# Kernel optimization log

Measured on AMD Instinct MI355X. Metric: run time of the kernel, lower is better.

The kernel has to match this reference:

```python
import jax, jax.numpy as jnp
import numpy as np

B, D_IN, H, E, TOP_K, NUM_TASKS = 131072, 512, 256, 8, 2, 1


def setup_inputs() -> dict:
    key = jax.random.key(0)
    ks = jax.random.split(key, 14)
    s = 0.02
    return {
        "x": jax.random.normal(ks[0], (B, D_IN), jnp.float32),
        "W_in": jax.random.normal(ks[1], (D_IN, H), jnp.float32) * s,
        "b_in": jnp.zeros((H,), jnp.float32),
        "W1": jax.random.normal(ks[2], (E, H, H), jnp.float32) * s,
        "b1": jnp.zeros((E, H), jnp.float32),
        "W2": jax.random.normal(ks[3], (E, H, H), jnp.float32) * s,
        "b2": jnp.zeros((E, H), jnp.float32),
        "Wg": jax.random.normal(ks[4], (H, E), jnp.float32) * s,
        "bg": jnp.zeros((E,), jnp.float32),
        "Wh1": jax.random.normal(ks[5], (H, H // 2), jnp.float32) * s,
        "bh1": jnp.zeros((H // 2,), jnp.float32),
        "Wh2": jax.random.normal(ks[6], (H // 2, NUM_TASKS), jnp.float32) * s,
        "bh2": jnp.zeros((NUM_TASKS,), jnp.float32),
    }


def reference(x, W_in, b_in, W1, b1, W2, b2, Wg, bg, Wh1, bh1, Wh2, bh2):
    h = x @ W_in + b_in                                   # [B, H]
    gates = jax.nn.softmax(h @ Wg + bg, axis=-1)          # [B, E]
    top_g, top_i = jax.lax.top_k(gates, TOP_K)            # [B, K]
    top_g = top_g / jnp.sum(top_g, axis=-1, keepdims=True)
    # dense all-expert compute (faithful to the original torch.stack)
    e1 = jax.nn.relu(jnp.einsum('bh,ehk->bek', h, W1) + b1)   # [B, E, H]
    eo = jnp.einsum('bek,ekh->beh', e1, W2) + b2              # [B, E, H]
    sel = jnp.take_along_axis(eo, top_i[:, :, None], axis=1)  # [B, K, H]
    out = jnp.einsum('bk,bkh->bh', top_g, sel)                # [B, H]
    y = jax.nn.relu(out @ Wh1 + bh1)                          # [B, H/2]
    return y @ Wh2 + bh2                                      # [B, num_tasks]
```

## Files before the change

kernel.cpp:

```cpp
#include <hip/hip_runtime.h>
#include <stdint.h>


#define NB 131072
#define DIN 512
#define HD 256

typedef short s16x8 __attribute__((ext_vector_type(8)));
typedef float f32x4 __attribute__((ext_vector_type(4)));

__device__ __forceinline__ unsigned short f2bf(float f) {
  uint32_t u = __builtin_bit_cast(uint32_t, f);
  u += 0x7FFFu + ((u >> 16) & 1u);
  return (unsigned short)(u >> 16);
}
__device__ __forceinline__ float bf2f(unsigned short s) {
  uint32_t u = ((uint32_t)s) << 16;
  return __builtin_bit_cast(float, u);
}

__global__ void k_prep_t(const float* __restrict__ Win, const float* __restrict__ W1,
                         const float* __restrict__ W2, const float* __restrict__ Wh1,
                         unsigned short* wt_in, unsigned short* w1t,
                         unsigned short* w2t, unsigned short* wh1t) {
  const int total = 131072 + 524288 + 524288 + 32768;
  for (int idx = blockIdx.x * 256 + threadIdx.x; idx < total; idx += gridDim.x * 256) {
    if (idx < 131072) {
      int n = idx >> 9, d = idx & 511;
      wt_in[idx] = f2bf(Win[d * 256 + n]);
    } else if (idx < 655360) {
      int i = idx - 131072;
      int e = i >> 16, n = (i >> 8) & 255, k = i & 255;
      w1t[i] = f2bf(W1[(e * 256 + k) * 256 + n]);
    } else if (idx < 1179648) {
      int i = idx - 655360;
      int e = i >> 16, n = (i >> 8) & 255, k = i & 255;
      w2t[i] = f2bf(W2[(e * 256 + k) * 256 + n]);
    } else {
      int i = idx - 1179648;
      int j = i >> 8, h = i & 255;
      wh1t[i] = f2bf(Wh1[h * 128 + j]);
    }
  }
}

__global__ void k_prep_gate(const float* __restrict__ Win, const float* __restrict__ Wg,
                            const float* __restrict__ b_in, const float* __restrict__ bg,
                            double* wf, double* bfv) {
  int t = blockIdx.x * 256 + threadIdx.x;
  if (t < 4096) {
    int d = t >> 3, e = t & 7;
    double acc = 0.0;
    for (int h = 0; h < 256; ++h)
      acc += (double)Win[d * 256 + h] * (double)Wg[h * 8 + e];
    wf[t] = acc;
  }
  if (blockIdx.x == 0 && threadIdx.x < 8) {
    int e = threadIdx.x;
    double acc = (double)bg[e];
    for (int h = 0; h < 256; ++h) acc += (double)b_in[h] * (double)Wg[h * 8 + e];
    bfv[e] = acc;
  }
}

__global__ __launch_bounds__(512) void k_hg(const float* __restrict__ x,
                                            const unsigned short* __restrict__ wt_in,
                                            const float* __restrict__ b_in,
                                            const double* __restrict__ wf,
                                            const double* __restrict__ bfv,
                                            unsigned short* __restrict__ hbuf,
                                            float2* __restrict__ g12,
                                            unsigned int* __restrict__ eidx) {
  __shared__ unsigned short xt[128 * 264];
  __shared__ double wfld[4 * 1026];
  const int tid = threadIdx.x;
  const int lane = tid & 63, wid = tid >> 6;
  const int wr = wid >> 2, wc = wid & 3;
  const int row0 = blockIdx.x * 128;

  for (int i = tid; i < 4096; i += 512)
    wfld[(i >> 10) * 1026 + (i & 1023)] = wf[i];

  f32x4 acc[4][4];
#pragma unroll
  for (int mi = 0; mi < 4; ++mi)
#pragma unroll
    for (int ni = 0; ni < 4; ++ni) acc[mi][ni] = (f32x4)0.0f;

  const int arow = wr * 64 + (lane & 15);
  const int bcol0 = wc * 64 + (lane & 15);
  const int koff = (lane >> 4) * 8;

  for (int ks = 0; ks < 2; ++ks) {
    __syncthreads();
#pragma unroll
    for (int i = 0; i < 8; ++i) {
      int flat = tid + i * 512;
      int r = flat >> 5, c8 = flat & 31;
      const float* src = x + (size_t)(row0 + r) * 512 + ks * 256 + c8 * 8;
      f32x4 v0 = *(const f32x4*)src;
      f32x4 v1 = *(const f32x4*)(src + 4);
      s16x8 sv;
      sv[0] = (short)f2bf(v0[0]); sv[1] = (short)f2bf(v0[1]);
      sv[2] = (short)f2bf(v0[2]); sv[3] = (short)f2bf(v0[3]);
      sv[4] = (short)f2bf(v1[0]); sv[5] = (short)f2bf(v1[1]);
      sv[6] = (short)f2bf(v1[2]); sv[7] = (short)f2bf(v1[3]);
      *(s16x8*)&xt[r * 264 + c8 * 8] = sv;
    }
    __syncthreads();
#pragma unroll
    for (int kk = 0; kk < 8; ++kk) {
      int k0 = kk * 32 + koff;
      s16x8 af[4], bfr[4];
#pragma unroll
      for (int mi = 0; mi < 4; ++mi)
        af[mi] = *(const s16x8*)&xt[(arow + mi * 16) * 264 + k0];
#pragma unroll
      for (int ni = 0; ni < 4; ++ni)
        bfr[ni] = *(const s16x8*)(wt_in + (size_t)(bcol0 + ni * 16) * 512 + ks * 256 + k0);
#pragma unroll
      for (int mi = 0; mi < 4; ++mi)
#pragma unroll
        for (int ni = 0; ni < 4; ++ni)
          acc[mi][ni] = __builtin_amdgcn_mfma_f32_16x16x32_bf16(af[mi], bfr[ni], acc[mi][ni], 0, 0, 0);
    }
  }
  const int r4 = (lane >> 4) * 4;
#pragma unroll
  for (int ni = 0; ni < 4; ++ni) {
    int col = wc * 64 + ni * 16 + (lane & 15);
    float bin = b_in[col];
#pragma unroll
    for (int mi = 0; mi < 4; ++mi) {
      int rbase = row0 + wr * 64 + mi * 16 + r4;
#pragma unroll
      for (int j = 0; j < 4; ++j)
        hbuf[(size_t)(rbase + j) * 256 + col] = f2bf(acc[mi][ni][j] + bin);
    }
  }

  const int r = tid >> 2, q = tid & 3;
  double z[8];
#pragma unroll
  for (int e = 0; e < 8; ++e) z[e] = 0.0;
  const float* xrow = x + (size_t)(row0 + r) * 512 + q * 128;
  const double* wq = &wfld[q * 1026];
  for (int dd = 0; dd < 32; ++dd) {
    f32x4 xv = *(const f32x4*)(xrow + dd * 4);
#pragma unroll
    for (int j = 0; j < 4; ++j) {
      double xd = (double)xv[j];
      const double* wrow = wq + (dd * 4 + j) * 8;
#pragma unroll
      for (int e = 0; e < 8; ++e) z[e] += xd * wrow[e];
    }
  }
#pragma unroll
  for (int e = 0; e < 8; ++e) {
    z[e] += __shfl_xor(z[e], 1);
    z[e] += __shfl_xor(z[e], 2);
  }
  if (q == 0) {
#pragma unroll
    for (int e = 0; e < 8; ++e) z[e] += bfv[e];
    int i1 = 0; double m1 = z[0];
#pragma unroll
    for (int e = 1; e < 8; ++e) if (z[e] > m1) { m1 = z[e]; i1 = e; }
    int i2 = -1; double m2 = -1e300;
#pragma unroll
    for (int e = 0; e < 8; ++e) if (e != i1 && z[e] > m2) { m2 = z[e]; i2 = e; }
    double s = exp(m2 - m1);
    int token = row0 + r;
    g12[token] = make_float2((float)(1.0 / (1.0 + s)), (float)(s / (1.0 + s)));
    eidx[token] = (unsigned)(i1 | (i2 << 4));
  }
}

__global__ __launch_bounds__(256) void k_hist(const unsigned int* __restrict__ eidx,
                                              unsigned int* __restrict__ bhist) {
  __shared__ unsigned int wcnt[4][8];
  const int tid = threadIdx.x;
  const int w = tid >> 6, lane = tid & 63;
  unsigned v = eidx[blockIdx.x * 256 + tid];
  int i1 = (int)(v & 15u), i2 = (int)((v >> 4) & 15u);
#pragma unroll
  for (int e = 0; e < 8; ++e) {
    unsigned long long m0 = __ballot(i1 == e);
    unsigned long long m1 = __ballot(i2 == e);
    if (lane == 0) wcnt[w][e] = (unsigned)(__popcll(m0) + __popcll(m1));
  }
  __syncthreads();
  if (tid < 8)
    bhist[blockIdx.x * 8 + tid] =
        wcnt[0][tid] + wcnt[1][tid] + wcnt[2][tid] + wcnt[3][tid];
}

__global__ __launch_bounds__(512) void k_scan1(const unsigned int* __restrict__ bhist,
                                               unsigned int* __restrict__ bbase,
                                               unsigned int* __restrict__ meta) {
  __shared__ unsigned int tot[8];
  const int tid = threadIdx.x;
  const int e = tid >> 6, lane = tid & 63;
  unsigned run = 0;
  for (int c = 0; c < 8; ++c) {
    int b = c * 64 + lane;
    unsigned v = bhist[b * 8 + e];
    unsigned s = v;
#pragma unroll
    for (int d = 1; d < 64; d <<= 1) {
      unsigned t2 = __shfl_up(s, d);
      if (lane >= d) s += t2;
    }
    bbase[b * 8 + e] = run + s - v;
    run += (unsigned)__shfl(s, 63);
  }
  if (lane == 63) tot[e] = run;
  __syncthreads();
  if (tid == 0) {
    unsigned bb = 0;
    for (int i = 0; i < 8; ++i) {
      meta[i] = bb;
      meta[16 + i] = tot[i];
      meta[32 + i] = bb * 64u;
      bb += (tot[i] + 63u) >> 6;
    }
    meta[8] = bb;
  }
}

__global__ __launch_bounds__(256) void k_scatter2(const unsigned int* __restrict__ eidx,
                                                  const unsigned int* __restrict__ bbase,
                                                  const unsigned int* __restrict__ meta,
                                                  unsigned int* __restrict__ perm) {
  __shared__ unsigned int wcnt[4][8];
  const int tid = threadIdx.x;
  const int w = tid >> 6, lane = tid & 63;
  const int t = blockIdx.x * 256 + tid;
  unsigned v = eidx[t];
  int i1 = (int)(v & 15u), i2 = (int)((v >> 4) & 15u);
  unsigned long long m0[8], m1[8];
#pragma unroll
  for (int e = 0; e < 8; ++e) {
    m0[e] = __ballot(i1 == e);
    m1[e] = __ballot(i2 == e);
    if (lane == 0) wcnt[w][e] = (unsigned)(__popcll(m0[e]) + __popcll(m1[e]));
  }
  __syncthreads();
  const unsigned long long below = (1ull << lane) - 1ull;
#pragma unroll
  for (int e = 0; e < 8; ++e) {
    unsigned base = meta[32 + e] + bbase[blockIdx.x * 8 + e];
    for (int w2 = 0; w2 < w; ++w2) base += wcnt[w2][e];
    if (i1 == e) {
      unsigned r = (unsigned)__popcll(m0[e] & below);
      perm[base + r] = (unsigned)(t * 2);
    }
    if (i2 == e) {
      unsigned r = (unsigned)__popcll(m0[e]) + (unsigned)__popcll(m1[e] & below);
      perm[base + r] = (unsigned)(t * 2 + 1);
    }
  }
}

__global__ __launch_bounds__(512) void k_expert(const unsigned short* __restrict__ hbuf,
                                                const unsigned short* __restrict__ w1t,
                                                const unsigned short* __restrict__ w2t,
                                                const unsigned short* __restrict__ wh1t,
                                                const float* __restrict__ b1,
                                                const float* __restrict__ b2,
                                                const unsigned int* __restrict__ meta,
                                                const unsigned int* __restrict__ perm,
                                                unsigned short* __restrict__ proj) {
  __shared__ unsigned short xt[64 * 264];
  __shared__ int ptok[64];
  const int b = blockIdx.x;
  if (b >= (int)meta[8]) return;
  int e = 0;
  while (e < 7 && (int)meta[e + 1] <= b) ++e;
  const int limit = (int)(meta[e] * 64u + meta[16 + e]);
  const int row0 = b * 64;
  const int tid = threadIdx.x;
  if (tid < 64) {
    int r = row0 + tid;
    ptok[tid] = (r < limit) ? (int)perm[r] : -1;
  }
  __syncthreads();
#pragma unroll
  for (int i = 0; i < 4; ++i) {
    int flat = tid + i * 512;
    int r = flat >> 5, c8 = flat & 31;
    int pt = ptok[r];
    s16x8 v = (s16x8)(short)0;
    if (pt >= 0) {
      int token = pt >> 1;
      v = *(const s16x8*)(hbuf + (size_t)token * 256 + c8 * 8);
    }
    *(s16x8*)&xt[r * 264 + c8 * 8] = v;
  }
  __syncthreads();

  const int lane = tid & 63, wid = tid >> 6;
  const int arow = lane & 15;
  const int koff = (lane >> 4) * 8;
  const int r4 = (lane >> 4) * 4;
  const int colb = wid * 32 + (lane & 15);

  f32x4 acc[4][2];
#pragma unroll
  for (int mi = 0; mi < 4; ++mi) { acc[mi][0] = (f32x4)0.0f; acc[mi][1] = (f32x4)0.0f; }
  const unsigned short* w1e = w1t + (size_t)e * 65536;
#pragma unroll
  for (int kk = 0; kk < 8; ++kk) {
    int k0 = kk * 32 + koff;
    s16x8 af[4], bfr[2];
#pragma unroll
    for (int mi = 0; mi < 4; ++mi)
      af[mi] = *(const s16x8*)&xt[(arow + mi * 16) * 264 + k0];
#pragma unroll
    for (int ni = 0; ni < 2; ++ni)
      bfr[ni] = *(const s16x8*)(w1e + (size_t)(colb + ni * 16) * 256 + k0);
#pragma unroll
    for (int mi = 0; mi < 4; ++mi)
#pragma unroll
      for (int ni = 0; ni < 2; ++ni)
        acc[mi][ni] = __builtin_amdgcn_mfma_f32_16x16x32_bf16(af[mi], bfr[ni], acc[mi][ni], 0, 0, 0);
  }
  __syncthreads();
#pragma unroll
  for (int ni = 0; ni < 2; ++ni) {
    int col = colb + ni * 16;
    float bb1 = b1[e * 256 + col];
#pragma unroll
    for (int mi = 0; mi < 4; ++mi) {
      int rl = mi * 16 + r4;
#pragma unroll
      for (int j = 0; j < 4; ++j) {
        float v = acc[mi][ni][j] + bb1;
        v = v > 0.f ? v : 0.f;
        xt[(rl + j) * 264 + col] = f2bf(v);
      }
    }
  }
  __syncthreads();

#pragma unroll
  for (int mi = 0; mi < 4; ++mi) { acc[mi][0] = (f32x4)0.0f; acc[mi][1] = (f32x4)0.0f; }
  const unsigned short* w2e = w2t + (size_t)e * 65536;
#pragma unroll
  for (int kk = 0; kk < 8; ++kk) {
    int k0 = kk * 32 + koff;
    s16x8 af[4], bfr[2];
#pragma unroll
    for (int mi = 0; mi < 4; ++mi)
      af[mi] = *(const s16x8*)&xt[(arow + mi * 16) * 264 + k0];
#pragma unroll
    for (int ni = 0; ni < 2; ++ni)
      bfr[ni] = *(const s16x8*)(w2e + (size_t)(colb + ni * 16) * 256 + k0);
#pragma unroll
    for (int mi = 0; mi < 4; ++mi)
#pragma unroll
      for (int ni = 0; ni < 2; ++ni)
        acc[mi][ni] = __builtin_amdgcn_mfma_f32_16x16x32_bf16(af[mi], bfr[ni], acc[mi][ni], 0, 0, 0);
  }
  __syncthreads();
#pragma unroll
  for (int ni = 0; ni < 2; ++ni) {
    int col = colb + ni * 16;
    float bb2 = b2[e * 256 + col];
#pragma unroll
    for (int mi = 0; mi < 4; ++mi) {
      int rl = mi * 16 + r4;
#pragma unroll
      for (int j = 0; j < 4; ++j)
        xt[(rl + j) * 264 + col] = f2bf(acc[mi][ni][j] + bb2);
    }
  }
  __syncthreads();

  f32x4 acc3[4];
#pragma unroll
  for (int mi = 0; mi < 4; ++mi) acc3[mi] = (f32x4)0.0f;
  const int col3 = wid * 16 + (lane & 15);
#pragma unroll
  for (int kk = 0; kk < 8; ++kk) {
    int k0 = kk * 32 + koff;
    s16x8 af[4];
#pragma unroll
    for (int mi = 0; mi < 4; ++mi)
      af[mi] = *(const s16x8*)&xt[(arow + mi * 16) * 264 + k0];
    s16x8 bfr = *(const s16x8*)(wh1t + (size_t)col3 * 256 + k0);
#pragma unroll
    for (int mi = 0; mi < 4; ++mi)
      acc3[mi] = __builtin_amdgcn_mfma_f32_16x16x32_bf16(af[mi], bfr, acc3[mi], 0, 0, 0);
  }
#pragma unroll
  for (int mi = 0; mi < 4; ++mi) {
#pragma unroll
    for (int j = 0; j < 4; ++j) {
      int rl = mi * 16 + r4 + j;
      int pt = ptok[rl];
      if (pt >= 0)
        proj[(size_t)pt * 128 + col3] = f2bf(acc3[mi][j]);
    }
  }
}

__global__ __launch_bounds__(256) void k_head(const unsigned short* __restrict__ proj,
                                              const float2* __restrict__ g12,
                                              const float* __restrict__ bh1,
                                              const float* __restrict__ wh2,
                                              const float* __restrict__ bh2,
                                              float* __restrict__ out) {
  __shared__ float sbh1[128];
  __shared__ float swh2[128];
  const int tid = threadIdx.x;
  if (tid < 128) { sbh1[tid] = bh1[tid]; swh2[tid] = wh2[tid]; }
  __syncthreads();
  const int token = blockIdx.x * 128 + (tid >> 1);
  const int half = tid & 1;
  const int j0 = half * 64;
  float2 g = g12[token];
  const unsigned short* p1 = proj + (size_t)token * 256 + j0;
  const unsigned short* p2 = p1 + 128;
  float sum = 0.f;
#pragma unroll
  for (int c = 0; c < 8; ++c) {
    s16x8 a = *(const s16x8*)(p1 + c * 8);
    s16x8 b = *(const s16x8*)(p2 + c * 8);
#pragma unroll
    for (int jj = 0; jj < 8; ++jj) {
      int j = j0 + c * 8 + jj;
      float v = g.x * bf2f((unsigned short)a[jj]) + g.y * bf2f((unsigned short)b[jj]) + sbh1[j];
      v = fmaxf(v, 0.f);
      sum += v * swh2[j];
    }
  }
  sum += __shfl_xor(sum, 1);
  if (half == 0) out[token] = sum + bh2[0];
}

extern "C" void kernel_launch(void* const* d_in, const int* in_sizes, int n_in,
                              void* d_out, int out_size, void* d_ws, size_t ws_size,
                              hipStream_t stream) {
  const float* x   = (const float*)d_in[0];
  const float* Win = (const float*)d_in[1];
  const float* bin = (const float*)d_in[2];
  const float* W1  = (const float*)d_in[3];
  const float* b1  = (const float*)d_in[4];
  const float* W2  = (const float*)d_in[5];
  const float* b2  = (const float*)d_in[6];
  const float* Wg  = (const float*)d_in[7];
  const float* bg  = (const float*)d_in[8];
  const float* Wh1 = (const float*)d_in[9];
  const float* bh1 = (const float*)d_in[10];
  const float* Wh2 = (const float*)d_in[11];
  const float* bh2 = (const float*)d_in[12];

  char* ws = (char*)d_ws;
  size_t o = 0;
  auto alloc = [&](size_t n) { o = (o + 255) & ~(size_t)255; void* p = ws + o; o += n; return p; };
  unsigned short* wt_in = (unsigned short*)alloc(262144);
  unsigned short* w1t   = (unsigned short*)alloc(1048576);
  unsigned short* w2t   = (unsigned short*)alloc(1048576);
  unsigned short* wh1t  = (unsigned short*)alloc(65536);
  double*        wf     = (double*)alloc(32768);
  double*        bfv    = (double*)alloc(64);
  unsigned short* hbuf  = (unsigned short*)alloc((size_t)NB * 256 * 2);
  float2*        g12    = (float2*)alloc((size_t)NB * 8);
  unsigned int*  eidx   = (unsigned int*)alloc((size_t)NB * 4);
  unsigned int*  bhist  = (unsigned int*)alloc(512 * 8 * 4);
  unsigned int*  bbase  = (unsigned int*)alloc(512 * 8 * 4);
  unsigned int*  meta   = (unsigned int*)alloc(256);
  unsigned int*  perm   = (unsigned int*)alloc(((size_t)NB * 2 + 2048) * 4);
  unsigned short* proj  = (unsigned short*)alloc((size_t)NB * 2 * 128 * 2);
  (void)ws_size; (void)in_sizes; (void)n_in; (void)out_size;

  k_prep_t<<<2048, 256, 0, stream>>>(Win, W1, W2, Wh1, wt_in, w1t, w2t, wh1t);
  k_prep_gate<<<16, 256, 0, stream>>>(Win, Wg, bin, bg, wf, bfv);
  k_hg<<<NB / 128, 512, 0, stream>>>(x, wt_in, bin, wf, bfv, hbuf, g12, eidx);
  k_hist<<<NB / 256, 256, 0, stream>>>(eidx, bhist);
  k_scan1<<<1, 512, 0, stream>>>(bhist, bbase, meta);
  k_scatter2<<<NB / 256, 256, 0, stream>>>(eidx, bbase, meta, perm);
  k_expert<<<NB * 2 / 64 + 8, 512, 0, stream>>>(hbuf, w1t, w2t, wh1t, b1, b2, meta, perm, proj);
  k_head<<<NB / 128, 256, 0, stream>>>(proj, g12, bh1, (const float*)Wh2, bh2, (float*)d_out);
}
```

Before: 420.9 us.

## Halve k_hg row tile and spread gate dot-products across 32 lanes per token

k_hg now handles 64 rows per block instead of 128. Each of the 8 waves computes a 64x32 column strip of h rather than a 64x64 tile in a 2x4 wave grid. The fp64 gate logits are now split across 32 lanes per token, each covering 16 input dims, with a 5-step shuffle reduction; before, 4 lanes split 128 dims each in a long serial loop. This doubles the grid and shortens the serial fp64 chain and its register use. In exchange, each block reloads more of the W_in fragments from global memory per row, and the wf table is staged to shared memory twice as often.

```diff
diff --git a/kernel.cpp b/kernel.cpp
--- a/kernel.cpp
+++ b/kernel.cpp
@@ -71,30 +71,27 @@
                                             unsigned short* __restrict__ hbuf,
                                             float2* __restrict__ g12,
                                             unsigned int* __restrict__ eidx) {
-  __shared__ unsigned short xt[128 * 264];
-  __shared__ double wfld[4 * 1026];
+  __shared__ unsigned short xt[64 * 264];
+  __shared__ double wfld[32 * 131];
   const int tid = threadIdx.x;
   const int lane = tid & 63, wid = tid >> 6;
-  const int wr = wid >> 2, wc = wid & 3;
-  const int row0 = blockIdx.x * 128;
+  const int row0 = blockIdx.x * 64;
 
   for (int i = tid; i < 4096; i += 512)
-    wfld[(i >> 10) * 1026 + (i & 1023)] = wf[i];
-
-  f32x4 acc[4][4];
-#pragma unroll
-  for (int mi = 0; mi < 4; ++mi)
-#pragma unroll
-    for (int ni = 0; ni < 4; ++ni) acc[mi][ni] = (f32x4)0.0f;
-
-  const int arow = wr * 64 + (lane & 15);
-  const int bcol0 = wc * 64 + (lane & 15);
+    wfld[(i >> 7) * 131 + (i & 127)] = wf[i];
+
+  const int arow = lane & 15;
+  const int colb = wid * 32 + (lane & 15);
   const int koff = (lane >> 4) * 8;
+  const int r4 = (lane >> 4) * 4;
+  f32x4 acc[4][2];
+#pragma unroll
+  for (int mi = 0; mi < 4; ++mi) { acc[mi][0] = (f32x4)0.0f; acc[mi][1] = (f32x4)0.0f; }
 
   for (int ks = 0; ks < 2; ++ks) {
     __syncthreads();
 #pragma unroll
-    for (int i = 0; i < 8; ++i) {
+    for (int i = 0; i < 4; ++i) {
       int flat = tid + i * 512;
       int r = flat >> 5, c8 = flat & 31;
       const float* src = x + (size_t)(row0 + r) * 512 + ks * 256 + c8 * 8;
@@ -111,68 +108,95 @@
 #pragma unroll
     for (int kk = 0; kk < 8; ++kk) {
       int k0 = kk * 32 + koff;
-      s16x8 af[4], bfr[4];
+      s16x8 af[4], bfr[2];
 #pragma unroll
       for (int mi = 0; mi < 4; ++mi)
         af[mi] = *(const s16x8*)&xt[(arow + mi * 16) * 264 + k0];
 #pragma unroll
-      for (int ni = 0; ni < 4; ++ni)
-        bfr[ni] = *(const s16x8*)(wt_in + (size_t)(bcol0 + ni * 16) * 512 + ks * 256 + k0);
+      for (int ni = 0; ni < 2; ++ni)
+        bfr[ni] = *(const s16x8*)(wt_in + (size_t)(colb + ni * 16) * 512 + ks * 256 + k0);
 #pragma unroll
       for (int mi = 0; mi < 4; ++mi)
 #pragma unroll
-        for (int ni = 0; ni < 4; ++ni)
+        for (int ni = 0; ni < 2; ++ni)
           acc[mi][ni] = __builtin_amdgcn_mfma_f32_16x16x32_bf16(af[mi], bfr[ni], acc[mi][ni], 0, 0, 0);
     }
   }
-  const int r4 = (lane >> 4) * 4;
-#pragma unroll
-  for (int ni = 0; ni < 4; ++ni) {
-    int col = wc * 64 + ni * 16 + (lane & 15);
+#pragma unroll
+  for (int ni = 0; ni < 2; ++ni) {
+    int col = colb + ni * 16;
     float bin = b_in[col];
 #pragma unroll
     for (int mi = 0; mi < 4; ++mi) {
-      int rbase = row0 + wr * 64 + mi * 16 + r4;
+      int rbase = row0 + mi * 16 + r4;
 #pragma unroll
       for (int j = 0; j < 4; ++j)
         hbuf[(size_t)(rbase + j) * 256 + col] = f2bf(acc[mi][ni][j] + bin);
     }
   }
 
-  const int r = tid >> 2, q = tid & 3;
-  double z[8];
-#pragma unroll
-  for (int e = 0; e < 8; ++e) z[e] = 0.0;
-  const float* xrow = x + (size_t)(row0 + r) * 512 + q * 128;
-  const double* wq = &wfld[q * 1026];
-  for (int dd = 0; dd < 32; ++dd) {
-    f32x4 xv = *(const f32x4*)(xrow + dd * 4);
-#pragma unroll
-    for (int j = 0; j < 4; ++j) {
-      double xd = (double)xv[j];
-      const double* wrow = wq + (dd * 4 + j) * 8;
-#pragma unroll
-      for (int e = 0; e < 8; ++e) z[e] += xd * wrow[e];
-    }
-  }
-#pragma unroll
-  for (int e = 0; e < 8; ++e) {
-    z[e] += __shfl_xor(z[e], 1);
-    z[e] += __shfl_xor(z[e], 2);
-  }
-  if (q == 0) {
-#pragma unroll
-    for (int e = 0; e < 8; ++e) z[e] += bfv[e];
-    int i1 = 0; double m1 = z[0];
-#pragma unroll
-    for (int e = 1; e < 8; ++e) if (z[e] > m1) { m1 = z[e]; i1 = e; }
-    int i2 = -1; double m2 = -1e300;
-#pragma unroll
-    for (int e = 0; e < 8; ++e) if (e != i1 && z[e] > m2) { m2 = z[e]; i2 = e; }
-    double s = exp(m2 - m1);
-    int token = row0 + r;
-    g12[token] = make_float2((float)(1.0 / (1.0 + s)), (float)(s / (1.0 + s)));
-    eidx[token] = (unsigned)(i1 | (i2 << 4));
+  const int q = tid & 31, g = tid >> 5;
+  const double* wq = &wfld[q * 131];
+#pragma unroll
+  for (int p = 0; p < 2; ++p) {
+    const int ta = g + p * 32;
+    const int tb = ta + 16;
+    const float* xa = x + (size_t)(row0 + ta) * 512 + q * 16;
+    const float* xb = x + (size_t)(row0 + tb) * 512 + q * 16;
+    double za[8], zb[8];
+#pragma unroll
+    for (int e = 0; e < 8; ++e) { za[e] = 0.0; zb[e] = 0.0; }
+#pragma unroll
+    for (int c = 0; c < 4; ++c) {
+      f32x4 va = *(const f32x4*)(xa + c * 4);
+      f32x4 vb = *(const f32x4*)(xb + c * 4);
+#pragma unroll
+      for (int j = 0; j < 4; ++j) {
+        const double* wrow = wq + (c * 4 + j) * 8;
+        double da = (double)va[j], db = (double)vb[j];
+#pragma unroll
+        for (int e = 0; e < 8; ++e) {
+          za[e] += da * wrow[e];
+          zb[e] += db * wrow[e];
+        }
+      }
+    }
+#pragma unroll
+    for (int e = 0; e < 8; ++e) {
+      za[e] += __shfl_xor(za[e], 1);  zb[e] += __shfl_xor(zb[e], 1);
+      za[e] += __shfl_xor(za[e], 2);  zb[e] += __shfl_xor(zb[e], 2);
+      za[e] += __shfl_xor(za[e], 4);  zb[e] += __shfl_xor(zb[e], 4);
+      za[e] += __shfl_xor(za[e], 8);  zb[e] += __shfl_xor(zb[e], 8);
+      za[e] += __shfl_xor(za[e], 16); zb[e] += __shfl_xor(zb[e], 16);
+    }
+    if (q == 0) {
+#pragma unroll
+      for (int e = 0; e < 8; ++e) { za[e] += bfv[e]; zb[e] += bfv[e]; }
+      {
+        int i1 = 0; double m1 = za[0];
+#pragma unroll
+        for (int e = 1; e < 8; ++e) if (za[e] > m1) { m1 = za[e]; i1 = e; }
+        int i2 = -1; double m2 = -1e300;
+#pragma unroll
+        for (int e = 0; e < 8; ++e) if (e != i1 && za[e] > m2) { m2 = za[e]; i2 = e; }
+        double s = exp(m2 - m1);
+        int token = row0 + ta;
+        g12[token] = make_float2((float)(1.0 / (1.0 + s)), (float)(s / (1.0 + s)));
+        eidx[token] = (unsigned)(i1 | (i2 << 4));
+      }
+      {
+        int i1 = 0; double m1 = zb[0];
+#pragma unroll
+        for (int e = 1; e < 8; ++e) if (zb[e] > m1) { m1 = zb[e]; i1 = e; }
+        int i2 = -1; double m2 = -1e300;
+#pragma unroll
+        for (int e = 0; e < 8; ++e) if (e != i1 && zb[e] > m2) { m2 = zb[e]; i2 = e; }
+        double s = exp(m2 - m1);
+        int token = row0 + tb;
+        g12[token] = make_float2((float)(1.0 / (1.0 + s)), (float)(s / (1.0 + s)));
+        eidx[token] = (unsigned)(i1 | (i2 << 4));
+      }
+    }
   }
 }
 
@@ -477,7 +501,7 @@
 
   k_prep_t<<<2048, 256, 0, stream>>>(Win, W1, W2, Wh1, wt_in, w1t, w2t, wh1t);
   k_prep_gate<<<16, 256, 0, stream>>>(Win, Wg, bin, bg, wf, bfv);
-  k_hg<<<NB / 128, 512, 0, stream>>>(x, wt_in, bin, wf, bfv, hbuf, g12, eidx);
+  k_hg<<<NB / 64, 512, 0, stream>>>(x, wt_in, bin, wf, bfv, hbuf, g12, eidx);
   k_hist<<<NB / 256, 256, 0, stream>>>(eidx, bhist);
   k_scan1<<<1, 512, 0, stream>>>(bhist, bbase, meta);
   k_scatter2<<<NB / 256, 256, 0, stream>>>(eidx, bbase, meta, perm);
```

New measurement: 449.8 us. 6.9% more time.

## Halve k_hg row tile and redistribute fp64 gate dot across lanes

Applied to the files above, without the earlier changes.

The input-projection kernel now processes 64 rows per block instead of 128, with each of the 8 waves computing a 64x32 column slab. This halves the LDS footprint and doubles the grid for better occupancy. The fp64 gate-logit computation drops the LDS staging of wf and reads it directly from global/L2 with vectorized f64x4 loads. Each token's 512-dim dot is split across 32 lanes with a 5-step shuffle reduction, replacing the old 4 lanes with a 2-step reduction. In exchange, wt_in is re-read by twice as many blocks and each wave reuses its B fragments over fewer rows.

```diff
diff --git a/kernel.cpp b/kernel.cpp
--- a/kernel.cpp
+++ b/kernel.cpp
@@ -8,6 +8,7 @@
 
 typedef short s16x8 __attribute__((ext_vector_type(8)));
 typedef float f32x4 __attribute__((ext_vector_type(4)));
+typedef double f64x4 __attribute__((ext_vector_type(4)));
 
 __device__ __forceinline__ unsigned short f2bf(float f) {
   uint32_t u = __builtin_bit_cast(uint32_t, f);
@@ -71,30 +72,23 @@
                                             unsigned short* __restrict__ hbuf,
                                             float2* __restrict__ g12,
                                             unsigned int* __restrict__ eidx) {
-  __shared__ unsigned short xt[128 * 264];
-  __shared__ double wfld[4 * 1026];
+  __shared__ unsigned short xt[64 * 264];
   const int tid = threadIdx.x;
   const int lane = tid & 63, wid = tid >> 6;
-  const int wr = wid >> 2, wc = wid & 3;
-  const int row0 = blockIdx.x * 128;
-
-  for (int i = tid; i < 4096; i += 512)
-    wfld[(i >> 10) * 1026 + (i & 1023)] = wf[i];
-
-  f32x4 acc[4][4];
-#pragma unroll
-  for (int mi = 0; mi < 4; ++mi)
-#pragma unroll
-    for (int ni = 0; ni < 4; ++ni) acc[mi][ni] = (f32x4)0.0f;
-
-  const int arow = wr * 64 + (lane & 15);
-  const int bcol0 = wc * 64 + (lane & 15);
+  const int row0 = blockIdx.x * 64;
+
+  const int arow = lane & 15;
+  const int colb = wid * 32 + (lane & 15);
   const int koff = (lane >> 4) * 8;
+  const int r4 = (lane >> 4) * 4;
+  f32x4 acc[4][2];
+#pragma unroll
+  for (int mi = 0; mi < 4; ++mi) { acc[mi][0] = (f32x4)0.0f; acc[mi][1] = (f32x4)0.0f; }
 
   for (int ks = 0; ks < 2; ++ks) {
     __syncthreads();
 #pragma unroll
-    for (int i = 0; i < 8; ++i) {
+    for (int i = 0; i < 4; ++i) {
       int flat = tid + i * 512;
       int r = flat >> 5, c8 = flat & 31;
       const float* src = x + (size_t)(row0 + r) * 512 + ks * 256 + c8 * 8;
@@ -111,68 +105,79 @@
 #pragma unroll
     for (int kk = 0; kk < 8; ++kk) {
       int k0 = kk * 32 + koff;
-      s16x8 af[4], bfr[4];
+      s16x8 af[4], bfr[2];
 #pragma unroll
       for (int mi = 0; mi < 4; ++mi)
         af[mi] = *(const s16x8*)&xt[(arow + mi * 16) * 264 + k0];
 #pragma unroll
-      for (int ni = 0; ni < 4; ++ni)
-        bfr[ni] = *(const s16x8*)(wt_in + (size_t)(bcol0 + ni * 16) * 512 + ks * 256 + k0);
+      for (int ni = 0; ni < 2; ++ni)
+        bfr[ni] = *(const s16x8*)(wt_in + (size_t)(colb + ni * 16) * 512 + ks * 256 + k0);
 #pragma unroll
       for (int mi = 0; mi < 4; ++mi)
 #pragma unroll
-        for (int ni = 0; ni < 4; ++ni)
+        for (int ni = 0; ni < 2; ++ni)
           acc[mi][ni] = __builtin_amdgcn_mfma_f32_16x16x32_bf16(af[mi], bfr[ni], acc[mi][ni], 0, 0, 0);
     }
   }
-  const int r4 = (lane >> 4) * 4;
-#pragma unroll
-  for (int ni = 0; ni < 4; ++ni) {
-    int col = wc * 64 + ni * 16 + (lane & 15);
+#pragma unroll
+  for (int ni = 0; ni < 2; ++ni) {
+    int col = colb + ni * 16;
     float bin = b_in[col];
 #pragma unroll
     for (int mi = 0; mi < 4; ++mi) {
-      int rbase = row0 + wr * 64 + mi * 16 + r4;
+      int rbase = row0 + mi * 16 + r4;
 #pragma unroll
       for (int j = 0; j < 4; ++j)
         hbuf[(size_t)(rbase + j) * 256 + col] = f2bf(acc[mi][ni][j] + bin);
     }
   }
 
-  const int r = tid >> 2, q = tid & 3;
-  double z[8];
-#pragma unroll
-  for (int e = 0; e < 8; ++e) z[e] = 0.0;
-  const float* xrow = x + (size_t)(row0 + r) * 512 + q * 128;
-  const double* wq = &wfld[q * 1026];
-  for (int dd = 0; dd < 32; ++dd) {
-    f32x4 xv = *(const f32x4*)(xrow + dd * 4);
-#pragma unroll
-    for (int j = 0; j < 4; ++j) {
-      double xd = (double)xv[j];
-      const double* wrow = wq + (dd * 4 + j) * 8;
-#pragma unroll
-      for (int e = 0; e < 8; ++e) z[e] += xd * wrow[e];
-    }
-  }
-#pragma unroll
-  for (int e = 0; e < 8; ++e) {
-    z[e] += __shfl_xor(z[e], 1);
-    z[e] += __shfl_xor(z[e], 2);
-  }
-  if (q == 0) {
-#pragma unroll
-    for (int e = 0; e < 8; ++e) z[e] += bfv[e];
-    int i1 = 0; double m1 = z[0];
-#pragma unroll
-    for (int e = 1; e < 8; ++e) if (z[e] > m1) { m1 = z[e]; i1 = e; }
-    int i2 = -1; double m2 = -1e300;
-#pragma unroll
-    for (int e = 0; e < 8; ++e) if (e != i1 && z[e] > m2) { m2 = z[e]; i2 = e; }
-    double s = exp(m2 - m1);
-    int token = row0 + r;
-    g12[token] = make_float2((float)(1.0 / (1.0 + s)), (float)(s / (1.0 + s)));
-    eidx[token] = (unsigned)(i1 | (i2 << 4));
+  const int q = tid & 31, g = tid >> 5;
+  const double* wq = wf + q * 16 * 8;
+#pragma unroll
+  for (int p = 0; p < 4; ++p) {
+    const int tok = g + p * 16;
+    const float* xr = x + (size_t)(row0 + tok) * 512 + q * 16;
+    double z[8];
+#pragma unroll
+    for (int e = 0; e < 8; ++e) z[e] = 0.0;
+#pragma unroll
+    for (int c = 0; c < 4; ++c) {
+      f32x4 xv = *(const f32x4*)(xr + c * 4);
+#pragma unroll
+      for (int j = 0; j < 4; ++j) {
+        const double* wrow = wq + (c * 4 + j) * 8;
+        f64x4 w0 = *(const f64x4*)(wrow);
+        f64x4 w1 = *(const f64x4*)(wrow + 4);
+        double xd = (double)xv[j];
+        z[0] += xd * w0[0]; z[1] += xd * w0[1];
+        z[2] += xd * w0[2]; z[3] += xd * w0[3];
+        z[4] += xd * w1[0]; z[5] += xd * w1[1];
+        z[6] += xd * w1[2]; z[7] += xd * w1[3];
+      }
+    }
+#pragma unroll
+    for (int e = 0; e < 8; ++e) {
+      z[e] += __shfl_xor(z[e], 1);
+      z[e] += __shfl_xor(z[e], 2);
+      z[e] += __shfl_xor(z[e], 4);
+      z[e] += __shfl_xor(z[e], 8);
+      z[e] += __shfl_xor(z[e], 16);
+    }
+    if (q == 0) {
+#pragma unroll
+      for (int e = 0; e < 8; ++e) z[e] += bfv[e];
+      int i1 = 0; double m1 = z[0];
+#pragma unroll
+      for (int e = 1; e < 8; ++e) if (z[e] > m1) { m1 = z[e]; i1 = e; }
+      int i2 = -1; double m2 = -1e300;
+#pragma unroll
+      for (int e = 0; e < 8; ++e) if (e != i1 && z[e] > m2) { m2 = z[e]; i2 = e; }
+      double s = exp(m2 - m1);
+      int token = row0 + tok;
+      g12[token] = make_float2((float)(1.0 / (1.0 + s)), (float)(s / (1.0 + s)));
+      eidx[token] = (unsigned)(i1 | (i2 << 4));
+    }
   }
 }
 
@@ -477,7 +482,7 @@
 
   k_prep_t<<<2048, 256, 0, stream>>>(Win, W1, W2, Wh1, wt_in, w1t, w2t, wh1t);
   k_prep_gate<<<16, 256, 0, stream>>>(Win, Wg, bin, bg, wf, bfv);
-  k_hg<<<NB / 128, 512, 0, stream>>>(x, wt_in, bin, wf, bfv, hbuf, g12, eidx);
+  k_hg<<<NB / 64, 512, 0, stream>>>(x, wt_in, bin, wf, bfv, hbuf, g12, eidx);
   k_hist<<<NB / 256, 256, 0, stream>>>(eidx, bhist);
   k_scan1<<<1, 512, 0, stream>>>(bhist, bbase, meta);
   k_scatter2<<<NB / 256, 256, 0, stream>>>(eidx, bbase, meta, perm);
```

After: 807.2 us. 1.92x slower.
